# Kernel tuning notes

Hardware: AMD Instinct MI355X
Metric: run time of the kernel (lower is better)

## Reference

```python
import jax, jax.numpy as jnp
import numpy as np

B, T, C = 2, 2048, 2048
H, G = 32, 8
D = C // H  # 64


def _rope_freqs(t, d_half, theta=10000.0):
    inv = 1.0 / (theta ** (np.arange(0, d_half, dtype=np.float32) / d_half * 2.0 / 2.0 * 2.0))
    # standard: freqs_i = theta^(-2i/D) for i in [0, D/2)
    inv = 1.0 / (theta ** (2.0 * np.arange(d_half, dtype=np.float32) / (2 * d_half)))
    ang = np.outer(np.arange(t, dtype=np.float32), inv)  # [T, D/2]
    return jnp.asarray(np.cos(ang)), jnp.asarray(np.sin(ang))


def setup_inputs() -> dict:
    key = jax.random.key(0)
    ks = jax.random.split(key, 5)
    s = 0.02
    cos, sin = _rope_freqs(T, D // 2)
    return {
        "x": jax.random.normal(ks[0], (B, T, C), jnp.float32),
        "freqs_cos": cos,
        "freqs_sin": sin,
        "mask": jnp.ones((1, 1), jnp.bool_),  # non-None mask -> causal attention
        "Wq": jax.random.normal(ks[1], (C, C), jnp.float32) * s,
        "Wk": jax.random.normal(ks[2], (C, G * D), jnp.float32) * s,
        "Wv": jax.random.normal(ks[3], (C, G * D), jnp.float32) * s,
        "Wo": jax.random.normal(ks[4], (C, C), jnp.float32) * s,
    }


def _apply_rope(x, cos, sin):
    # x: [B, T, N, D]; pairs (x[..., 2i], x[..., 2i+1]) rotated by angle[t, i]
    b, t, n, d = x.shape
    xr = x.astype(jnp.float32).reshape(b, t, n, d // 2, 2)
    x0, x1 = xr[..., 0], xr[..., 1]
    c = cos[:t][None, :, None, :]
    s = sin[:t][None, :, None, :]
    out = jnp.stack([x0 * c - x1 * s, x0 * s + x1 * c], axis=-1)
    return out.reshape(b, t, n, d).astype(x.dtype)


def reference(x, freqs_cos, freqs_sin, mask, Wq, Wk, Wv, Wo):
    b, t, c = x.shape
    q = (x @ Wq).reshape(b, t, H, D)
    k = (x @ Wk).reshape(b, t, G, D)
    v = (x @ Wv).reshape(b, t, G, D)
    q = _apply_rope(q, freqs_cos, freqs_sin)
    k = _apply_rope(k, freqs_cos, freqs_sin)
    k_cache, v_cache = k, v  # new_kv_cache (pre-expansion)
    # GQA expansion: repeat_interleave along head dim
    rep = H // G
    ke = jnp.repeat(k, rep, axis=2)  # [B, T, H, D]
    ve = jnp.repeat(v, rep, axis=2)
    scale = 1.0 / jnp.sqrt(jnp.asarray(D, x.dtype))
    scores = jnp.einsum("bqhd,bkhd->bhqk", q, ke) * scale  # [B, H, T, T]
    causal = jnp.tril(jnp.ones((t, t), jnp.bool_))
    scores = jnp.where(causal[None, None], scores, jnp.finfo(scores.dtype).min)
    attn = jax.nn.softmax(scores, axis=-1)
    out = jnp.einsum("bhqk,bkhd->bqhd", attn, ve).reshape(b, t, c)
    return out @ Wo, k_cache, v_cache
```

## Files before the change

kernel.cpp:

```cpp
#include <hip/hip_runtime.h>
#include <cstdint>
#include <cstddef>

typedef unsigned short ushort_t;
typedef __attribute__((ext_vector_type(4))) float f32x4;
typedef __attribute__((ext_vector_type(16))) float f32x16;
typedef __attribute__((ext_vector_type(8))) short short8;
typedef __attribute__((ext_vector_type(4))) float float4_t;
typedef __attribute__((ext_vector_type(4))) unsigned short ushort4_t;
typedef __attribute__((ext_vector_type(2))) unsigned int uint2v;

#define KD 2048
#define TT 2048
#define NH 32
#define NG 8

__device__ __forceinline__ ushort_t f2bf(float f) {
  union { float f; uint32_t u; } cv; cv.f = f;
  uint32_t u = cv.u;
  return (ushort_t)((u + 0x7FFFu + ((u >> 16) & 1u)) >> 16);
}

__device__ __forceinline__ uint32_t cvtpk(float a, float b) {
  uint32_t r;
  asm("v_cvt_pk_bf16_f32 %0, %1, %2" : "=v"(r) : "v"(a), "v"(b));
  return r;
}

__device__ __forceinline__ float exp2fast(float x) {
  float r;
  asm("v_exp_f32 %0, %1" : "=v"(r) : "v"(x));
  return r;
}

__device__ __forceinline__ void gload_lds16(const void* g, void* l) {
  __builtin_amdgcn_global_load_lds(
      (const __attribute__((address_space(1))) unsigned int*)g,
      (__attribute__((address_space(3))) unsigned int*)l, 16, 0, 0);
}

__global__ __launch_bounds__(256) void cvt_x_kernel(const float* __restrict__ src,
                                                    ushort_t* __restrict__ dst) {
  int i = (blockIdx.x * 256 + threadIdx.x) * 4;
  float4_t v = *(const float4_t*)(src + i);
  ushort4_t o;
  o[0] = f2bf(v[0]); o[1] = f2bf(v[1]); o[2] = f2bf(v[2]); o[3] = f2bf(v[3]);
  *(ushort4_t*)(dst + i) = o;
}

__global__ __launch_bounds__(256) void cvt_wt_kernel(const float* __restrict__ Wq,
                                                     const float* __restrict__ Wk,
                                                     const float* __restrict__ Wv,
                                                     const float* __restrict__ Wo,
                                                     ushort_t* __restrict__ wqkvT,
                                                     ushort_t* __restrict__ woT) {
  __shared__ float tile[32][33];
  const int bid = blockIdx.x;
  const float* src;
  ushort_t* dst;
  int Nc, bx, by;
  if (bid < 4096)      { src = Wq; dst = wqkvT;                       Nc = 2048; int r = bid;        bx = r & 63; by = r >> 6; }
  else if (bid < 5120) { src = Wk; dst = wqkvT + (size_t)2048 * KD;   Nc = 512;  int r = bid - 4096; bx = r & 15; by = r >> 4; }
  else if (bid < 6144) { src = Wv; dst = wqkvT + (size_t)2560 * KD;   Nc = 512;  int r = bid - 5120; bx = r & 15; by = r >> 4; }
  else                 { src = Wo; dst = woT;                         Nc = 2048; int r = bid - 6144; bx = r & 63; by = r >> 6; }
  const int tx = threadIdx.x, ty = threadIdx.y;
  const int c0 = bx * 32, r0 = by * 32;
#pragma unroll
  for (int i = 0; i < 4; i++)
    tile[ty + i * 8][tx] = src[(size_t)(r0 + ty + i * 8) * Nc + c0 + tx];
  __syncthreads();
#pragma unroll
  for (int i = 0; i < 4; i++)
    dst[(size_t)(c0 + ty + i * 8) * KD + r0 + tx] = f2bf(tile[tx][ty + i * 8]);
}

__global__ __launch_bounds__(256) void vtrans_kernel(const ushort_t* __restrict__ v,
                                                     ushort_t* __restrict__ vt) {
  __shared__ ushort_t tile[64][72];
  const int bg = blockIdx.y;
  const int t0 = blockIdx.x * 64;
  const ushort_t* src = v + ((size_t)bg * TT + t0) * 64;
#pragma unroll
  for (int i = 0; i < 2; ++i) {
    int p = i * 256 + threadIdx.x;
    int r = p >> 3, c = (p & 7) * 8;
    *(short8*)&tile[r][c] = *(const short8*)(src + r * 64 + c);
  }
  __syncthreads();
  ushort_t* dst = vt + (size_t)bg * 64 * TT + t0;
#pragma unroll
  for (int i = 0; i < 2; ++i) {
    int p = i * 256 + threadIdx.x;
    int d = p >> 3, c = (p & 7) * 8;
    short8 o;
#pragma unroll
    for (int j = 0; j < 8; ++j) o[j] = tile[c + j][d];
    *(short8*)(dst + (size_t)d * TT + c) = o;
  }
}

template <int MODE, int BN, int WM>
__global__ __launch_bounds__(512) void gemmr_kernel(
    const ushort_t* __restrict__ A, const ushort_t* __restrict__ Bt,
    const float* __restrict__ cosT, const float* __restrict__ sinT,
    ushort_t* __restrict__ q_ws, ushort_t* __restrict__ k_ws,
    ushort_t* __restrict__ v_ws, float* __restrict__ kcache,
    float* __restrict__ vcache, float* __restrict__ outF) {
  constexpr int NT = KD / 64;
  constexpr int WN = 8 / WM;
  constexpr int RW = 256 / WM;
  constexpr int CW = BN / WN;
  constexpr int MF = RW / 16;
  constexpr int NF = CW / 16;
  constexpr int MQ = MF / 2;
  constexpr int BL = BN / 64;
  constexpr int ASZ = 256 * 64;
  constexpr int BSZ = BN * 64;
  __shared__ ushort_t sA[3 * ASZ];
  __shared__ ushort_t sB[2 * BSZ];
  const int tid = threadIdx.x;
  const int lane = tid & 63;
  const int w = tid >> 6;
  const int wm = (WM == 2) ? (w >> 2) : (w >> 1);
  const int wn = (WM == 2) ? (w & 3) : (w & 1);
  const int bid = blockIdx.x;
  const int j = bid >> 3;
  const int by = 2 * (bid & 7) + (j & 1);
  const int bx = j >> 1;
  const int rowBase = by * 256;
  const int colBase = bx * BN;

  int aRO[4], aLO[4];
#pragma unroll
  for (int i = 0; i < 4; ++i) {
    int c = i * 512 + tid;
    int r = c >> 3, lc = (c & 7) ^ (r & 7);
    aRO[i] = r * KD + lc * 8;
    aLO[i] = (i * 512 + (tid & ~63)) * 8;
  }
  int bRO[BL], bLO[BL];
#pragma unroll
  for (int i = 0; i < BL; ++i) {
    int c = i * 512 + tid;
    int r = c >> 3, lc = (c & 7) ^ (r & 7);
    bRO[i] = r * KD + lc * 8;
    bLO[i] = (i * 512 + (tid & ~63)) * 8;
  }

  auto stageA = [&](int slot, int kt) {
    const ushort_t* base = A + (size_t)rowBase * KD + kt * 64;
#pragma unroll
    for (int i = 0; i < 4; ++i)
      gload_lds16(base + aRO[i], &sA[slot * ASZ + aLO[i]]);
  };
  auto stageB = [&](int bb, int kt) {
    const ushort_t* base = Bt + (size_t)colBase * KD + kt * 64;
#pragma unroll
    for (int i = 0; i < BL; ++i)
      gload_lds16(base + bRO[i], &sB[bb * BSZ + bLO[i]]);
  };

  f32x4 acc[MF][NF];
#pragma unroll
  for (int i = 0; i < MF; i++)
#pragma unroll
    for (int j2 = 0; j2 < NF; j2++) acc[i][j2] = f32x4{0.f, 0.f, 0.f, 0.f};

  stageA(0, 0); stageB(0, 0);
  stageA(1, 1); stageB(1, 1);
  asm volatile("s_waitcnt vmcnt(%0)" :: "n"(4 + BL) : "memory");
  __builtin_amdgcn_s_barrier();

  int am3 = 0;
  int sm3 = 2;
  for (int k = 0; k < NT; ++k) {
    const int bb = k & 1;
    const ushort_t* Abuf = &sA[am3 * ASZ];
    const ushort_t* Bbuf = &sB[bb * BSZ];

    short8 bfr[NF][2];
#pragma unroll
    for (int ni = 0; ni < NF; ++ni) {
      int n = wn * CW + ni * 16 + (lane & 15);
#pragma unroll
      for (int ks = 0; ks < 2; ++ks)
        bfr[ni][ks] = *(const short8*)(&Bbuf[n * 64 +
            (((ks * 4 + (lane >> 4)) ^ (n & 7)) * 8)]);
    }
    short8 af0[MQ][2];
#pragma unroll
    for (int mq = 0; mq < MQ; ++mq) {
      int r = wm * RW + mq * 16 + (lane & 15);
#pragma unroll
      for (int ks = 0; ks < 2; ++ks)
        af0[mq][ks] = *(const short8*)(&Abuf[r * 64 +
            (((ks * 4 + (lane >> 4)) ^ (r & 7)) * 8)]);
    }
    if (k + 2 < NT) stageA(sm3, k + 2);
    __builtin_amdgcn_s_barrier();
    __builtin_amdgcn_s_setprio(1);
#pragma unroll
    for (int ks = 0; ks < 2; ++ks)
#pragma unroll
      for (int mq = 0; mq < MQ; ++mq)
#pragma unroll
        for (int ni = 0; ni < NF; ++ni)
          acc[mq][ni] = __builtin_amdgcn_mfma_f32_16x16x32_bf16(
              af0[mq][ks], bfr[ni][ks], acc[mq][ni], 0, 0, 0);
    __builtin_amdgcn_s_setprio(0);
    __builtin_amdgcn_s_barrier();

    short8 af1[MQ][2];
#pragma unroll
    for (int mq = 0; mq < MQ; ++mq) {
      int r = wm * RW + (MQ + mq) * 16 + (lane & 15);
#pragma unroll
      for (int ks = 0; ks < 2; ++ks)
        af1[mq][ks] = *(const short8*)(&Abuf[r * 64 +
            (((ks * 4 + (lane >> 4)) ^ (r & 7)) * 8)]);
    }
    if (k + 2 < NT) stageB(bb, k + 2);
    __builtin_amdgcn_s_barrier();
    __builtin_amdgcn_s_setprio(1);
#pragma unroll
    for (int ks = 0; ks < 2; ++ks)
#pragma unroll
      for (int mq = 0; mq < MQ; ++mq)
#pragma unroll
        for (int ni = 0; ni < NF; ++ni)
          acc[MQ + mq][ni] = __builtin_amdgcn_mfma_f32_16x16x32_bf16(
              af1[mq][ks], bfr[ni][ks], acc[MQ + mq][ni], 0, 0, 0);
    __builtin_amdgcn_s_setprio(0);
    if (k + 2 < NT)
      asm volatile("s_waitcnt vmcnt(%0)" :: "n"(4 + BL) : "memory");
    else
      asm volatile("s_waitcnt vmcnt(0)" ::: "memory");
    __builtin_amdgcn_s_barrier();

    am3 = (am3 == 2) ? 0 : am3 + 1;
    sm3 = (sm3 == 2) ? 0 : sm3 + 1;
  }

#pragma unroll
  for (int mi = 0; mi < MF; ++mi)
#pragma unroll
    for (int ni = 0; ni < NF; ++ni) {
      int cg = colBase + wn * CW + ni * 16 + (lane & 15);
      int rg0 = rowBase + wm * RW + mi * 16 + ((lane >> 4) * 4);
      f32x4 v4 = acc[mi][ni];
#pragma unroll
      for (int j2 = 0; j2 < 4; ++j2) {
        float v = v4[j2];
        float pv = __shfl_xor(v, 1);
        int row = rg0 + j2;
        if constexpr (MODE == 0) {
          int bb2 = row >> 11, tq = row & (TT - 1);
          int d = cg & 63, i2 = d >> 1;
          if (cg < 2048) {
            float cc = cosT[tq * 32 + i2], ss = sinT[tq * 32 + i2];
            float out = (d & 1) ? (pv * ss + v * cc) : (v * cc - pv * ss);
            int hh = cg >> 6;
            q_ws[(((size_t)(bb2 * NH + hh)) * TT + tq) * 64 + d] = f2bf(out * 0.18033688f);
          } else if (cg < 2560) {
            float cc = cosT[tq * 32 + i2], ss = sinT[tq * 32 + i2];
            float out = (d & 1) ? (pv * ss + v * cc) : (v * cc - pv * ss);
            int gg = (cg - 2048) >> 6;
            kcache[(((size_t)(bb2 * TT + tq)) * NG + gg) * 64 + d] = out;
            k_ws[(((size_t)(bb2 * NG + gg)) * TT + tq) * 64 + d] = f2bf(out);
          } else {
            int gg = (cg - 2560) >> 6;
            vcache[(((size_t)(bb2 * TT + tq)) * NG + gg) * 64 + d] = v;
            v_ws[(((size_t)(bb2 * NG + gg)) * TT + tq) * 64 + d] = f2bf(v);
          }
        } else {
          outF[(size_t)row * 2048 + cg] = v;
        }
      }
    }
}

#define PACK(SV, E, OUT)                                        \
  {                                                             \
    uint32_t A0 = cvtpk(SV[8 * E + 0], SV[8 * E + 1]);          \
    uint32_t A1 = cvtpk(SV[8 * E + 2], SV[8 * E + 3]);          \
    uint32_t B0 = cvtpk(SV[8 * E + 4], SV[8 * E + 5]);          \
    uint32_t B1 = cvtpk(SV[8 * E + 6], SV[8 * E + 7]);          \
    asm("v_permlane32_swap_b32 %0, %1" : "+v"(A0), "+v"(B0));   \
    asm("v_permlane32_swap_b32 %0, %1" : "+v"(A1), "+v"(B1));   \
    union { uint32_t u[4]; short8 s8; } UU;                     \
    UU.u[0] = A0; UU.u[1] = A1; UU.u[2] = B0; UU.u[3] = B1;     \
    OUT = UU.s8;                                                \
  }

__global__ __launch_bounds__(256, 4) void attn_kernel(const ushort_t* __restrict__ qw,
                                                      const ushort_t* __restrict__ kw,
                                                      const ushort_t* __restrict__ vtw,
                                                      ushort_t* __restrict__ attn) {
  __shared__ ushort_t sK[2][4096];
  __shared__ ushort_t sVT[2][4096];
  const int tid = threadIdx.x;
  const int lane = tid & 63;
  const int w = tid >> 6;
  const int hi = lane >> 5;
  const int col = lane & 31;
  const int bid = blockIdx.x;
  const int j = bid >> 3;
  const int pair = 2 * (bid & 7) + (j & 1);
  const int b = pair >> 3, g = pair & 7;
  const int rep = (j >> 1) & 3;
  const int h = g * 4 + rep;
  const int qt = 15 - (j >> 3);
  const int q0w = qt * 128 + w * 32;
  const int qg = q0w + col;
  const int ntiles = 2 * qt + 2;

  const ushort_t* qbase = qw + ((size_t)(b * NH + h) * TT + qg) * 64;
  const ushort_t* kbase = kw + (size_t)(b * NG + g) * TT * 64;
  const ushort_t* vtbase = vtw + (size_t)(b * NG + g) * 64 * TT;

  short8 qf[4];
#pragma unroll
  for (int dsub = 0; dsub < 4; ++dsub)
    qf[dsub] = *(const short8*)(qbase + dsub * 16 + hi * 8);

  const int r0 = tid >> 3;
  const int cl = (tid & 7) ^ (r0 & 7);
  const ushort_t* kS0 = kbase + r0 * 64 + cl * 8;
  const ushort_t* kS1 = kbase + (r0 + 32) * 64 + cl * 8;
  const ushort_t* vS0 = vtbase + (size_t)r0 * TT + cl * 8;
  const ushort_t* vS1 = vtbase + (size_t)(r0 + 32) * TT + cl * 8;
  const int off0 = (tid & ~63) * 8;
  const int off1 = off0 + 2048;

  auto stage = [&](int bb, int k0) {
    gload_lds16(kS0 + (size_t)k0 * 64, &sK[bb][off0]);
    gload_lds16(kS1 + (size_t)k0 * 64, &sK[bb][off1]);
    gload_lds16(vS0 + k0, &sVT[bb][off0]);
    gload_lds16(vS1 + k0, &sVT[bb][off1]);
  };

  f32x16 o0 = {};
  f32x16 o1 = {};
  float m_run = -3.0e38f, l_run = 0.f;

  stage(0, 0);
  asm volatile("s_waitcnt vmcnt(0)" ::: "memory");
  __syncthreads();

  for (int kt = 0; kt < ntiles; ++kt) {
    const int k0 = kt * 64;
    const int buf = kt & 1;
    if (kt + 1 < ntiles) stage(buf ^ 1, k0 + 64);
    if (k0 <= q0w + 31) {
      const ushort_t* K = sK[buf];
      const ushort_t* V = sVT[buf];
      f32x16 s0 = {};
      f32x16 s1 = {};
#pragma unroll
      for (int dsub = 0; dsub < 4; ++dsub) {
        const int ch = dsub * 2 + hi;
        const int sw = ((ch ^ (col & 7)) * 8);
        short8 a0 = *(const short8*)(K + col * 64 + sw);
        short8 a1 = *(const short8*)(K + (32 + col) * 64 + sw);
        s0 = __builtin_amdgcn_mfma_f32_32x32x16_bf16(a0, qf[dsub], s0, 0, 0, 0);
        s1 = __builtin_amdgcn_mfma_f32_32x32x16_bf16(a1, qf[dsub], s1, 0, 0, 0);
      }
      if (k0 + 63 > q0w) {
#pragma unroll
        for (int r = 0; r < 16; ++r) {
          int key5 = (r & 3) + 8 * (r >> 2) + 4 * hi;
          if (k0 + key5 > qg) s0[r] = -3.0e38f;
          if (k0 + 32 + key5 > qg) s1[r] = -3.0e38f;
        }
      }
      float tm[16];
#pragma unroll
      for (int r = 0; r < 16; ++r) tm[r] = fmaxf(s0[r], s1[r]);
#pragma unroll
      for (int st = 8; st > 0; st >>= 1)
#pragma unroll
        for (int r = 0; r < 8; ++r)
          if (r < st) tm[r] = fmaxf(tm[r], tm[r + st]);
      float mt = fmaxf(tm[0], __shfl_xor(tm[0], 32));
      if (!__all(mt - m_run <= 8.0f)) {
        float mn = fmaxf(m_run, mt);
        float al = exp2fast(m_run - mn);
        m_run = mn;
        l_run *= al;
#pragma unroll
        for (int r = 0; r < 16; ++r) { o0[r] *= al; o1[r] *= al; }
      }
      float ts[16];
#pragma unroll
      for (int r = 0; r < 16; ++r) {
        s0[r] = exp2fast(s0[r] - m_run);
        s1[r] = exp2fast(s1[r] - m_run);
        ts[r] = s0[r] + s1[r];
      }
#pragma unroll
      for (int st = 8; st > 0; st >>= 1)
#pragma unroll
        for (int r = 0; r < 8; ++r)
          if (r < st) ts[r] += ts[r + st];
      float rs = ts[0] + __shfl_xor(ts[0], 32);
      l_run += rs;
      short8 pb;
      const int swz = (col & 7);
#define PVMM(KS)                                                            \
  {                                                                         \
    const int ch = KS * 2 + hi;                                             \
    const int so = ((ch ^ swz) * 8);                                        \
    short8 va = *(const short8*)(V + col * 64 + so);                        \
    short8 vb = *(const short8*)(V + (32 + col) * 64 + so);                 \
    o0 = __builtin_amdgcn_mfma_f32_32x32x16_bf16(va, pb, o0, 0, 0, 0);      \
    o1 = __builtin_amdgcn_mfma_f32_32x32x16_bf16(vb, pb, o1, 0, 0, 0);      \
  }
      PACK(s0, 0, pb); PVMM(0)
      PACK(s0, 1, pb); PVMM(1)
      PACK(s1, 0, pb); PVMM(2)
      PACK(s1, 1, pb); PVMM(3)
#undef PVMM
    }
    asm volatile("s_waitcnt vmcnt(0)" ::: "memory");
    __syncthreads();
  }

  const float inv = 1.f / l_run;
  ushort_t* obase = attn + ((size_t)b * TT + qg) * 2048 + h * 64;
#pragma unroll
  for (int g4 = 0; g4 < 4; ++g4) {
    int d = g4 * 8 + hi * 4;
    uint2v u;
    u[0] = cvtpk(o0[4 * g4 + 0] * inv, o0[4 * g4 + 1] * inv);
    u[1] = cvtpk(o0[4 * g4 + 2] * inv, o0[4 * g4 + 3] * inv);
    *(uint2v*)(obase + d) = u;
    uint2v u2;
    u2[0] = cvtpk(o1[4 * g4 + 0] * inv, o1[4 * g4 + 1] * inv);
    u2[1] = cvtpk(o1[4 * g4 + 2] * inv, o1[4 * g4 + 3] * inv);
    *(uint2v*)(obase + 32 + d) = u2;
  }
}

extern "C" void kernel_launch(void* const* d_in, const int* in_sizes, int n_in,
                              void* d_out, int out_size, void* d_ws, size_t ws_size,
                              hipStream_t stream) {
  (void)in_sizes; (void)n_in; (void)out_size; (void)ws_size;
  const float* x    = (const float*)d_in[0];
  const float* cosT = (const float*)d_in[1];
  const float* sinT = (const float*)d_in[2];
  const float* Wq   = (const float*)d_in[4];
  const float* Wk   = (const float*)d_in[5];
  const float* Wv   = (const float*)d_in[6];
  const float* Wo   = (const float*)d_in[7];

  float* outF   = (float*)d_out;
  float* kcache = outF + (size_t)8388608;
  float* vcache = kcache + (size_t)2097152;

  uint8_t* ws = (uint8_t*)d_ws;
  ushort_t* x_bf   = (ushort_t*)(ws);
  ushort_t* wqkvT  = (ushort_t*)(ws + 16777216);
  ushort_t* vt_ws  = (ushort_t*)(ws + 16777216);
  ushort_t* q_ws   = (ushort_t*)(ws + 29360128);
  ushort_t* k_ws   = (ushort_t*)(ws + 46137344);
  ushort_t* v_ws   = (ushort_t*)(ws + 50331648);
  ushort_t* woT    = (ushort_t*)(ws + 54525952);
  ushort_t* attn_ws= (ushort_t*)(ws + 62914560);

  cvt_x_kernel<<<8192, 256, 0, stream>>>(x, x_bf);
  cvt_wt_kernel<<<10240, dim3(32, 8), 0, stream>>>(Wq, Wk, Wv, Wo, wqkvT, woT);

  gemmr_kernel<0, 192, 2><<<256, 512, 0, stream>>>(x_bf, wqkvT, cosT, sinT,
                                                   q_ws, k_ws, v_ws, kcache,
                                                   vcache, nullptr);
  vtrans_kernel<<<dim3(32, 16), 256, 0, stream>>>(v_ws, vt_ws);
  attn_kernel<<<1024, 256, 0, stream>>>(q_ws, k_ws, vt_ws, attn_ws);
  gemmr_kernel<1, 128, 4><<<256, 512, 0, stream>>>(attn_ws, woT, nullptr,
                                                   nullptr, nullptr, nullptr,
                                                   nullptr, nullptr, nullptr,
                                                   outF);
}
```

Baseline: 188.7 us.

## Quantize QKV projection inputs to int8 and use int8 MFMA GEMM

Adds per-row int8 quantization of x (straight from fp32) and of the transposed QKV weights, each with its own row scale. A new int8 GEMM kernel built on 16x16x64 i8 MFMA, with 128-byte K tiles, replaces the bf16 QKV GEMM and applies the scales in the RoPE epilogue. The aim is to double MFMA throughput and halve operand bytes for the largest projection. The cost is an extra weight-quantization pass and a real loss of precision from int8 rounding, which may push outputs outside tolerance. The output-projection GEMM is simplified to a plain fp32 store, and the workspace layout is rearranged.

New measurement: 173.1 us. 1.09x faster.

```diff
diff --git a/kernel.cpp b/kernel.cpp
--- a/kernel.cpp
+++ b/kernel.cpp
@@ -3,12 +3,15 @@
 #include <cstddef>
 
 typedef unsigned short ushort_t;
+typedef signed char s8;
 typedef __attribute__((ext_vector_type(4))) float f32x4;
 typedef __attribute__((ext_vector_type(16))) float f32x16;
 typedef __attribute__((ext_vector_type(8))) short short8;
 typedef __attribute__((ext_vector_type(4))) float float4_t;
 typedef __attribute__((ext_vector_type(4))) unsigned short ushort4_t;
 typedef __attribute__((ext_vector_type(2))) unsigned int uint2v;
+typedef __attribute__((ext_vector_type(4))) int int4v;
+typedef __attribute__((ext_vector_type(2))) int int2v;
 
 #define KD 2048
 #define TT 2048
@@ -21,6 +24,11 @@
   return (ushort_t)((u + 0x7FFFu + ((u >> 16) & 1u)) >> 16);
 }
 
+__device__ __forceinline__ float bf2f(ushort_t v) {
+  union { uint32_t u; float f; } cv; cv.u = ((uint32_t)v) << 16;
+  return cv.f;
+}
+
 __device__ __forceinline__ uint32_t cvtpk(float a, float b) {
   uint32_t r;
   asm("v_cvt_pk_bf16_f32 %0, %1, %2" : "=v"(r) : "v"(a), "v"(b));
@@ -39,13 +47,57 @@
       (__attribute__((address_space(3))) unsigned int*)l, 16, 0, 0);
 }
 
-__global__ __launch_bounds__(256) void cvt_x_kernel(const float* __restrict__ src,
-                                                    ushort_t* __restrict__ dst) {
-  int i = (blockIdx.x * 256 + threadIdx.x) * 4;
-  float4_t v = *(const float4_t*)(src + i);
-  ushort4_t o;
-  o[0] = f2bf(v[0]); o[1] = f2bf(v[1]); o[2] = f2bf(v[2]); o[3] = f2bf(v[3]);
-  *(ushort4_t*)(dst + i) = o;
+__global__ __launch_bounds__(256) void xq_kernel(const float* __restrict__ x,
+                                                 s8* __restrict__ xq,
+                                                 float* __restrict__ xs) {
+  const int row = blockIdx.x;
+  const int tid = threadIdx.x;
+  const float* src = x + (size_t)row * 2048 + tid * 8;
+  float4_t a = *(const float4_t*)(src);
+  float4_t b = *(const float4_t*)(src + 4);
+  float m = fmaxf(fmaxf(fmaxf(fabsf(a[0]), fabsf(a[1])), fmaxf(fabsf(a[2]), fabsf(a[3]))),
+                  fmaxf(fmaxf(fabsf(b[0]), fabsf(b[1])), fmaxf(fabsf(b[2]), fabsf(b[3]))));
+#pragma unroll
+  for (int st = 32; st > 0; st >>= 1) m = fmaxf(m, __shfl_xor(m, st));
+  __shared__ float red[4];
+  if ((tid & 63) == 0) red[tid >> 6] = m;
+  __syncthreads();
+  m = fmaxf(fmaxf(red[0], red[1]), fmaxf(red[2], red[3]));
+  const float inv = (m > 0.f) ? 127.f / m : 0.f;
+  union { s8 c[8]; int2v v; } pk;
+#pragma unroll
+  for (int i = 0; i < 4; ++i) {
+    pk.c[i]     = (s8)__float2int_rn(a[i] * inv);
+    pk.c[4 + i] = (s8)__float2int_rn(b[i] * inv);
+  }
+  *(int2v*)(xq + (size_t)row * 2048 + tid * 8) = pk.v;
+  if (tid == 0) xs[row] = (m > 0.f) ? m / 127.f : 0.f;
+}
+
+__global__ __launch_bounds__(256) void wq_kernel(const ushort_t* __restrict__ wt,
+                                                 s8* __restrict__ wq,
+                                                 float* __restrict__ wqs) {
+  const int row = blockIdx.x;
+  const int tid = threadIdx.x;
+  short8 v8 = *(const short8*)(wt + (size_t)row * 2048 + tid * 8);
+  float f[8];
+#pragma unroll
+  for (int i = 0; i < 8; ++i) f[i] = bf2f((ushort_t)v8[i]);
+  float m = 0.f;
+#pragma unroll
+  for (int i = 0; i < 8; ++i) m = fmaxf(m, fabsf(f[i]));
+#pragma unroll
+  for (int st = 32; st > 0; st >>= 1) m = fmaxf(m, __shfl_xor(m, st));
+  __shared__ float red[4];
+  if ((tid & 63) == 0) red[tid >> 6] = m;
+  __syncthreads();
+  m = fmaxf(fmaxf(red[0], red[1]), fmaxf(red[2], red[3]));
+  const float inv = (m > 0.f) ? 127.f / m : 0.f;
+  union { s8 c[8]; int2v v; } pk;
+#pragma unroll
+  for (int i = 0; i < 8; ++i) pk.c[i] = (s8)__float2int_rn(f[i] * inv);
+  *(int2v*)(wq + (size_t)row * 2048 + tid * 8) = pk.v;
+  if (tid == 0) wqs[row] = (m > 0.f) ? m / 127.f : 0.f;
 }
 
 __global__ __launch_bounds__(256) void cvt_wt_kernel(const float* __restrict__ Wq,
@@ -99,13 +151,185 @@
   }
 }
 
-template <int MODE, int BN, int WM>
-__global__ __launch_bounds__(512) void gemmr_kernel(
-    const ushort_t* __restrict__ A, const ushort_t* __restrict__ Bt,
+__global__ __launch_bounds__(512) void gemmq_kernel(
+    const s8* __restrict__ A, const s8* __restrict__ Bt,
+    const float* __restrict__ xs, const float* __restrict__ wqs,
     const float* __restrict__ cosT, const float* __restrict__ sinT,
     ushort_t* __restrict__ q_ws, ushort_t* __restrict__ k_ws,
     ushort_t* __restrict__ v_ws, float* __restrict__ kcache,
-    float* __restrict__ vcache, float* __restrict__ outF) {
+    float* __restrict__ vcache) {
+  constexpr int NT = 16;
+  constexpr int RW = 128, CW = 48;
+  constexpr int MF = 8, NF = 3, MQ = 4, BL = 3;
+  constexpr int ASZ = 256 * 128;
+  constexpr int BSZ = 192 * 128;
+  __shared__ s8 sA[3 * ASZ];
+  __shared__ s8 sB[2 * BSZ];
+  const int tid = threadIdx.x;
+  const int lane = tid & 63;
+  const int w = tid >> 6;
+  const int wm = w >> 2, wn = w & 3;
+  const int bid = blockIdx.x;
+  const int j = bid >> 3;
+  const int by = 2 * (bid & 7) + (j & 1);
+  const int bx = j >> 1;
+  const int rowBase = by * 256;
+  const int colBase = bx * 192;
+
+  int aRO[4], aLO[4];
+#pragma unroll
+  for (int i = 0; i < 4; ++i) {
+    int c = i * 512 + tid;
+    int r = c >> 3, lc = (c & 7) ^ (r & 7);
+    aRO[i] = r * 2048 + lc * 16;
+    aLO[i] = (i * 512 + (tid & ~63)) * 16;
+  }
+  int bRO[BL], bLO[BL];
+#pragma unroll
+  for (int i = 0; i < BL; ++i) {
+    int c = i * 512 + tid;
+    int r = c >> 3, lc = (c & 7) ^ (r & 7);
+    bRO[i] = r * 2048 + lc * 16;
+    bLO[i] = (i * 512 + (tid & ~63)) * 16;
+  }
+
+  auto stageA = [&](int slot, int kt) {
+    const s8* base = A + (size_t)rowBase * 2048 + kt * 128;
+#pragma unroll
+    for (int i = 0; i < 4; ++i)
+      gload_lds16(base + aRO[i], &sA[slot * ASZ + aLO[i]]);
+  };
+  auto stageB = [&](int bb2, int kt) {
+    const s8* base = Bt + (size_t)colBase * 2048 + kt * 128;
+#pragma unroll
+    for (int i = 0; i < BL; ++i)
+      gload_lds16(base + bRO[i], &sB[bb2 * BSZ + bLO[i]]);
+  };
+
+  int4v acc[MF][NF];
+#pragma unroll
+  for (int i = 0; i < MF; i++)
+#pragma unroll
+    for (int j2 = 0; j2 < NF; j2++) acc[i][j2] = int4v{0, 0, 0, 0};
+
+  stageA(0, 0); stageB(0, 0);
+  stageA(1, 1); stageB(1, 1);
+  asm volatile("s_waitcnt vmcnt(%0)" :: "n"(4 + BL) : "memory");
+  __builtin_amdgcn_s_barrier();
+
+  int am3 = 0;
+  int sm3 = 2;
+  for (int k = 0; k < NT; ++k) {
+    const int bb = k & 1;
+    const s8* Abuf = &sA[am3 * ASZ];
+    const s8* Bbuf = &sB[bb * BSZ];
+
+    int4v bfr[NF][2];
+#pragma unroll
+    for (int ni = 0; ni < NF; ++ni) {
+      int n = wn * CW + ni * 16 + (lane & 15);
+#pragma unroll
+      for (int ks = 0; ks < 2; ++ks)
+        bfr[ni][ks] = *(const int4v*)(&Bbuf[n * 128 +
+            (((ks * 4 + (lane >> 4)) ^ (n & 7)) * 16)]);
+    }
+    int4v af0[MQ][2];
+#pragma unroll
+    for (int mq = 0; mq < MQ; ++mq) {
+      int r = wm * RW + mq * 16 + (lane & 15);
+#pragma unroll
+      for (int ks = 0; ks < 2; ++ks)
+        af0[mq][ks] = *(const int4v*)(&Abuf[r * 128 +
+            (((ks * 4 + (lane >> 4)) ^ (r & 7)) * 16)]);
+    }
+    if (k + 2 < NT) stageA(sm3, k + 2);
+    __builtin_amdgcn_s_barrier();
+    __builtin_amdgcn_s_setprio(1);
+#pragma unroll
+    for (int ks = 0; ks < 2; ++ks)
+#pragma unroll
+      for (int mq = 0; mq < MQ; ++mq)
+#pragma unroll
+        for (int ni = 0; ni < NF; ++ni)
+          acc[mq][ni] = __builtin_amdgcn_mfma_i32_16x16x64_i8(
+              af0[mq][ks], bfr[ni][ks], acc[mq][ni], 0, 0, 0);
+    __builtin_amdgcn_s_setprio(0);
+    __builtin_amdgcn_s_barrier();
+
+    int4v af1[MQ][2];
+#pragma unroll
+    for (int mq = 0; mq < MQ; ++mq) {
+      int r = wm * RW + (MQ + mq) * 16 + (lane & 15);
+#pragma unroll
+      for (int ks = 0; ks < 2; ++ks)
+        af1[mq][ks] = *(const int4v*)(&Abuf[r * 128 +
+            (((ks * 4 + (lane >> 4)) ^ (r & 7)) * 16)]);
+    }
+    if (k + 2 < NT) stageB(bb, k + 2);
+    __builtin_amdgcn_s_barrier();
+    __builtin_amdgcn_s_setprio(1);
+#pragma unroll
+    for (int ks = 0; ks < 2; ++ks)
+#pragma unroll
+      for (int mq = 0; mq < MQ; ++mq)
+#pragma unroll
+        for (int ni = 0; ni < NF; ++ni)
+          acc[MQ + mq][ni] = __builtin_amdgcn_mfma_i32_16x16x64_i8(
+              af1[mq][ks], bfr[ni][ks], acc[MQ + mq][ni], 0, 0, 0);
+    __builtin_amdgcn_s_setprio(0);
+    if (k + 2 < NT)
+      asm volatile("s_waitcnt vmcnt(%0)" :: "n"(4 + BL) : "memory");
+    else
+      asm volatile("s_waitcnt vmcnt(0)" ::: "memory");
+    __builtin_amdgcn_s_barrier();
+
+    am3 = (am3 == 2) ? 0 : am3 + 1;
+    sm3 = (sm3 == 2) ? 0 : sm3 + 1;
+  }
+
+#pragma unroll
+  for (int mi = 0; mi < MF; ++mi) {
+    int rg0 = rowBase + wm * RW + mi * 16 + ((lane >> 4) * 4);
+    float sar[4];
+#pragma unroll
+    for (int jj = 0; jj < 4; ++jj) sar[jj] = xs[rg0 + jj];
+#pragma unroll
+    for (int ni = 0; ni < NF; ++ni) {
+      int cg = colBase + wn * CW + ni * 16 + (lane & 15);
+      const float sb = wqs[cg];
+      int4v v4 = acc[mi][ni];
+#pragma unroll
+      for (int j2 = 0; j2 < 4; ++j2) {
+        float v = (float)v4[j2] * sar[j2] * sb;
+        float pv = __shfl_xor(v, 1);
+        int row = rg0 + j2;
+        int bb2 = row >> 11, tq = row & (TT - 1);
+        int d = cg & 63, i2 = d >> 1;
+        if (cg < 2048) {
+          float cc = cosT[tq * 32 + i2], ss = sinT[tq * 32 + i2];
+          float out = (d & 1) ? (pv * ss + v * cc) : (v * cc - pv * ss);
+          int hh = cg >> 6;
+          q_ws[(((size_t)(bb2 * NH + hh)) * TT + tq) * 64 + d] = f2bf(out * 0.18033688f);
+        } else if (cg < 2560) {
+          float cc = cosT[tq * 32 + i2], ss = sinT[tq * 32 + i2];
+          float out = (d & 1) ? (pv * ss + v * cc) : (v * cc - pv * ss);
+          int gg = (cg - 2048) >> 6;
+          kcache[(((size_t)(bb2 * TT + tq)) * NG + gg) * 64 + d] = out;
+          k_ws[(((size_t)(bb2 * NG + gg)) * TT + tq) * 64 + d] = f2bf(out);
+        } else {
+          int gg = (cg - 2560) >> 6;
+          vcache[(((size_t)(bb2 * TT + tq)) * NG + gg) * 64 + d] = v;
+          v_ws[(((size_t)(bb2 * NG + gg)) * TT + tq) * 64 + d] = f2bf(v);
+        }
+      }
+    }
+  }
+}
+
+template <int BN, int WM>
+__global__ __launch_bounds__(512) void gemmr_kernel(
+    const ushort_t* __restrict__ A, const ushort_t* __restrict__ Bt,
+    float* __restrict__ outF) {
   constexpr int NT = KD / 64;
   constexpr int WN = 8 / WM;
   constexpr int RW = 256 / WM;
@@ -153,11 +377,11 @@
     for (int i = 0; i < 4; ++i)
       gload_lds16(base + aRO[i], &sA[slot * ASZ + aLO[i]]);
   };
-  auto stageB = [&](int bb, int kt) {
+  auto stageB = [&](int bb2, int kt) {
     const ushort_t* base = Bt + (size_t)colBase * KD + kt * 64;
 #pragma unroll
     for (int i = 0; i < BL; ++i)
-      gload_lds16(base + bRO[i], &sB[bb * BSZ + bLO[i]]);
+      gload_lds16(base + bRO[i], &sB[bb2 * BSZ + bLO[i]]);
   };
 
   f32x4 acc[MF][NF];
@@ -249,33 +473,8 @@
       int rg0 = rowBase + wm * RW + mi * 16 + ((lane >> 4) * 4);
       f32x4 v4 = acc[mi][ni];
 #pragma unroll
-      for (int j2 = 0; j2 < 4; ++j2) {
-        float v = v4[j2];
-        float pv = __shfl_xor(v, 1);
-        int row = rg0 + j2;
-        if constexpr (MODE == 0) {
-          int bb2 = row >> 11, tq = row & (TT - 1);
-          int d = cg & 63, i2 = d >> 1;
-          if (cg < 2048) {
-            float cc = cosT[tq * 32 + i2], ss = sinT[tq * 32 + i2];
-            float out = (d & 1) ? (pv * ss + v * cc) : (v * cc - pv * ss);
-            int hh = cg >> 6;
-            q_ws[(((size_t)(bb2 * NH + hh)) * TT + tq) * 64 + d] = f2bf(out * 0.18033688f);
-          } else if (cg < 2560) {
-            float cc = cosT[tq * 32 + i2], ss = sinT[tq * 32 + i2];
-            float out = (d & 1) ? (pv * ss + v * cc) : (v * cc - pv * ss);
-            int gg = (cg - 2048) >> 6;
-            kcache[(((size_t)(bb2 * TT + tq)) * NG + gg) * 64 + d] = out;
-            k_ws[(((size_t)(bb2 * NG + gg)) * TT + tq) * 64 + d] = f2bf(out);
-          } else {
-            int gg = (cg - 2560) >> 6;
-            vcache[(((size_t)(bb2 * TT + tq)) * NG + gg) * 64 + d] = v;
-            v_ws[(((size_t)(bb2 * NG + gg)) * TT + tq) * 64 + d] = f2bf(v);
-          }
-        } else {
-          outF[(size_t)row * 2048 + cg] = v;
-        }
-      }
+      for (int j2 = 0; j2 < 4; ++j2)
+        outF[(size_t)(rg0 + j2) * 2048 + cg] = v4[j2];
     }
 }
 
@@ -287,9 +486,9 @@
     uint32_t B1 = cvtpk(SV[8 * E + 6], SV[8 * E + 7]);          \
     asm("v_permlane32_swap_b32 %0, %1" : "+v"(A0), "+v"(B0));   \
     asm("v_permlane32_swap_b32 %0, %1" : "+v"(A1), "+v"(B1));   \
-    union { uint32_t u[4]; short8 s8; } UU;                     \
+    union { uint32_t u[4]; short8 s8v; } UU;                    \
     UU.u[0] = A0; UU.u[1] = A1; UU.u[2] = B0; UU.u[3] = B1;     \
-    OUT = UU.s8;                                                \
+    OUT = UU.s8v;                                               \
   }
 
 __global__ __launch_bounds__(256, 4) void attn_kernel(const ushort_t* __restrict__ qw,
@@ -458,25 +657,25 @@
   float* vcache = kcache + (size_t)2097152;
 
   uint8_t* ws = (uint8_t*)d_ws;
-  ushort_t* x_bf   = (ushort_t*)(ws);
+  s8*       xq     = (s8*)(ws);
+  float*    xs     = (float*)(ws + 8388608);
+  float*    wqs    = (float*)(ws + 8388608 + 65536);
+  ushort_t* vt_ws  = (ushort_t*)(ws + 9437184);
   ushort_t* wqkvT  = (ushort_t*)(ws + 16777216);
-  ushort_t* vt_ws  = (ushort_t*)(ws + 16777216);
-  ushort_t* q_ws   = (ushort_t*)(ws + 29360128);
-  ushort_t* k_ws   = (ushort_t*)(ws + 46137344);
-  ushort_t* v_ws   = (ushort_t*)(ws + 50331648);
-  ushort_t* woT    = (ushort_t*)(ws + 54525952);
-  ushort_t* attn_ws= (ushort_t*)(ws + 62914560);
-
-  cvt_x_kernel<<<8192, 256, 0, stream>>>(x, x_bf);
+  ushort_t* attn_ws= (ushort_t*)(ws + 16777216);
+  s8*       wq_q   = (s8*)(ws + 35651584);
+  ushort_t* q_ws   = (ushort_t*)(ws + 41943040);
+  ushort_t* k_ws   = (ushort_t*)(ws + 58720256);
+  ushort_t* v_ws   = (ushort_t*)(ws + 62914560);
+  ushort_t* woT    = (ushort_t*)(ws + 67108864);
+
+  xq_kernel<<<4096, 256, 0, stream>>>(x, xq, xs);
   cvt_wt_kernel<<<10240, dim3(32, 8), 0, stream>>>(Wq, Wk, Wv, Wo, wqkvT, woT);
-
-  gemmr_kernel<0, 192, 2><<<256, 512, 0, stream>>>(x_bf, wqkvT, cosT, sinT,
-                                                   q_ws, k_ws, v_ws, kcache,
-                                                   vcache, nullptr);
+  wq_kernel<<<3072, 256, 0, stream>>>(wqkvT, wq_q, wqs);
+
+  gemmq_kernel<<<256, 512, 0, stream>>>(xq, wq_q, xs, wqs, cosT, sinT,
+                                        q_ws, k_ws, v_ws, kcache, vcache);
   vtrans_kernel<<<dim3(32, 16), 256, 0, stream>>>(v_ws, vt_ws);
   attn_kernel<<<1024, 256, 0, stream>>>(q_ws, k_ws, vt_ws, attn_ws);
-  gemmr_kernel<1, 128, 4><<<256, 512, 0, stream>>>(attn_ws, woT, nullptr,
-                                                   nullptr, nullptr, nullptr,
-                                                   nullptr, nullptr, nullptr,
-                                                   outF);
-}
+  gemmr_kernel<128, 4><<<256, 512, 0, stream>>>(attn_ws, woT, outF);
+}
```
